# Optimization experiments

Measured on AMD Instinct MI355X. Metric: run time of the kernel, lower is better.

The kernel has to match this reference:

```python
import jax, jax.numpy as jnp
import numpy as np

DIM = 512
BLOCK = 64
SPARSITY = 0.9
B, L = 4, 2048
NEG_INF = jnp.float32(-jnp.inf)


def _block_sparse_mask(key, seq_len, block_size, sparsity):
    # mirrors BasicQuantumAttention._get_block_sparse_mask, with diagonal
    # blocks forced on so no softmax row is fully masked (avoids NaNs)
    nb = (seq_len + block_size - 1) // block_size
    blk = jax.random.uniform(key, (nb, nb)) > sparsity
    blk = jnp.tril(blk) | jnp.eye(nb, dtype=bool)
    m = jnp.repeat(jnp.repeat(blk, block_size, axis=0), block_size, axis=1)
    return m[:seq_len, :seq_len]


def setup_inputs() -> dict:
    key = jax.random.key(0)
    ks = jax.random.split(key, 12)
    d = DIM
    inp = {}
    names = ['q_real', 'q_imag', 'k_real', 'k_imag', 'v_real', 'v_imag']
    for i, n in enumerate(names):
        inp[n] = jax.random.normal(ks[i], (B, L, d), dtype=jnp.float32)
    # xavier-ish init for Linear weights (torch Linear: y = x @ W.T + b)
    s6 = (2.0 / (6 * d + 6 * d)) ** 0.5
    s2 = (2.0 / (2 * d + 2 * d)) ** 0.5
    inp['W_qkv'] = jax.random.normal(ks[6], (6 * d, 6 * d), dtype=jnp.float32) * s6
    inp['b_qkv'] = jnp.zeros((6 * d,), dtype=jnp.float32)
    inp['W_out'] = jax.random.normal(ks[7], (2 * d, 2 * d), dtype=jnp.float32) * s2
    inp['b_out'] = jnp.zeros((2 * d,), dtype=jnp.float32)
    # two independent random block-sparse masks (one per stream, as in the
    # original which regenerates the mask inside each _chunk_attention call)
    inp['mask_real'] = _block_sparse_mask(ks[8], L, BLOCK, SPARSITY)
    inp['mask_imag'] = _block_sparse_mask(ks[9], L, BLOCK, SPARSITY)
    return inp


def _masked_attention(q, k, v, mask, scale):
    # q,k,v: [B,L,d]; mask: [L,L] bool (True = keep)
    scores = jnp.einsum('bqd,bkd->bqk', q, k) * scale
    scores = jnp.where(mask[None, :, :], scores, NEG_INF)
    attn = jax.nn.softmax(scores, axis=-1)  # dropout is identity in eval
    return jnp.einsum('bqk,bkd->bqd', attn, v)


def reference(q_real, q_imag, k_real, k_imag, v_real, v_imag,
              W_qkv, b_qkv, W_out, b_out, mask_real, mask_imag):
    d = q_real.shape[-1]
    scale = jnp.asarray(d, q_real.dtype) ** -0.5
    x = jnp.concatenate([q_real, q_imag, k_real, k_imag, v_real, v_imag], axis=-1)
    qkv = x @ W_qkv.T + b_qkv                       # [B,L,6d]
    q_r, q_i, k_r, k_i, v_r, v_i = jnp.split(qkv, 6, axis=-1)
    out_real = _masked_attention(q_r, k_r, v_r, mask_real, scale)
    out_imag = _masked_attention(q_i, k_i, v_i, mask_imag, scale)
    out = jnp.concatenate([out_real, out_imag], axis=-1)  # [B,L,2d]
    out = out @ W_out.T + b_out
    return out[..., :d], out[..., d:]
```

## Files before the change

### kernel.cpp

```cpp
#include <hip/hip_runtime.h>
#include <stdint.h>

typedef __attribute__((ext_vector_type(8))) short short8;
typedef __attribute__((ext_vector_type(4))) float f32x4;

#define DEV __device__ __forceinline__

DEV unsigned short f2bf(float f) {
    unsigned int u = __float_as_uint(f);
    u += 0x7FFFu + ((u >> 16) & 1u);
    return (unsigned short)(u >> 16);
}

DEV void gload_lds16(const void* g, void* l) {
    __builtin_amdgcn_global_load_lds(
        (const __attribute__((address_space(1))) unsigned int*)g,
        (__attribute__((address_space(3))) unsigned int*)l,
        16, 0, 0);
}

__global__ __launch_bounds__(256) void f32_to_bf16_k(
    const float* __restrict__ in, unsigned short* __restrict__ out, int n8) {
    int i = blockIdx.x * 256 + threadIdx.x;
    if (i >= n8) return;
    const float4* src = (const float4*)in + (size_t)i * 2;
    float4 a = src[0], b = src[1];
    short8 o;
    o[0] = f2bf(a.x); o[1] = f2bf(a.y); o[2] = f2bf(a.z); o[3] = f2bf(a.w);
    o[4] = f2bf(b.x); o[5] = f2bf(b.y); o[6] = f2bf(b.z); o[7] = f2bf(b.w);
    *((short8*)out + i) = o;
}

__global__ __launch_bounds__(256) void pack_x_k(
    const float* __restrict__ p0, const float* __restrict__ p1,
    const float* __restrict__ p2, const float* __restrict__ p3,
    const float* __restrict__ p4, const float* __restrict__ p5,
    unsigned short* __restrict__ x) {
    int i = blockIdx.x * 256 + threadIdx.x;
    int e0 = i * 8;
    int m = e0 / 3072;
    int k = e0 - m * 3072;
    int sel = k >> 9;
    const float* src;
    switch (sel) {
        case 0: src = p0; break; case 1: src = p1; break;
        case 2: src = p2; break; case 3: src = p3; break;
        case 4: src = p4; break; default: src = p5; break;
    }
    src += (size_t)m * 512 + (k & 511);
    float4 a = *(const float4*)src;
    float4 b = *(const float4*)(src + 4);
    short8 o;
    o[0] = f2bf(a.x); o[1] = f2bf(a.y); o[2] = f2bf(a.z); o[3] = f2bf(a.w);
    o[4] = f2bf(b.x); o[5] = f2bf(b.y); o[6] = f2bf(b.z); o[7] = f2bf(b.w);
    *(short8*)(x + e0) = o;
}

__global__ void scan_masks_k(const void* mr, const void* mi,
                             int* __restrict__ nact, unsigned char* __restrict__ lists) {
    int t = threadIdx.x;
    if (t >= 64) return;
    int s = t >> 5, qb = t & 31;
    const unsigned char* det = (const unsigned char*)mr;
    bool is_byte = det[1] != 0;
    const void* m = s ? mi : mr;
    int cnt = 0;
    for (int kb = 0; kb < 32; ++kb) {
        size_t off = (size_t)(qb * 64) * 2048 + (size_t)kb * 64;
        bool on = is_byte ? (((const unsigned char*)m)[off] != 0)
                          : (((const int*)m)[off] != 0);
        if (on) lists[t * 32 + cnt++] = (unsigned char)kb;
    }
    nact[t] = cnt;
}

template <int MODE>
__global__ __launch_bounds__(256, 2) void gemm_bt(
    const unsigned short* __restrict__ A, const unsigned short* __restrict__ B,
    const float* __restrict__ bias, unsigned short* __restrict__ Cb,
    float* __restrict__ Cf, int M, int N, int K, int halfN, int half_elems) {
    __shared__ unsigned short As[128 * 32];
    __shared__ unsigned short Bs[128 * 32];
    const int tid = threadIdx.x;
    const int wave = tid >> 6, lane = tid & 63;
    const int bm = blockIdx.x, bn = blockIdx.y;
    const int wr = wave >> 1, wc = wave & 1;
    const int fr = lane & 15, fo = lane >> 4;
    const int srow = lane >> 2;
    const int scol = (lane & 3) * 8;
    f32x4 acc[4][4];
    #pragma unroll
    for (int mi = 0; mi < 4; ++mi)
        #pragma unroll
        for (int ni = 0; ni < 4; ++ni) acc[mi][ni] = f32x4{0.f, 0.f, 0.f, 0.f};

    for (int k0 = 0; k0 < K; k0 += 32) {
        #pragma unroll
        for (int r = 0; r < 2; ++r) {
            int arow = bm * 128 + r * 64 + wave * 16 + srow;
            gload_lds16(A + (size_t)arow * K + k0 + scol,
                        As + (r * 64 + wave * 16) * 32);
            int brow = bn * 128 + r * 64 + wave * 16 + srow;
            gload_lds16(B + (size_t)brow * K + k0 + scol,
                        Bs + (r * 64 + wave * 16) * 32);
        }
        __syncthreads();
        short8 af[4], bfr[4];
        #pragma unroll
        for (int mi = 0; mi < 4; ++mi)
            af[mi] = *(const short8*)(As + (wr * 64 + mi * 16 + fr) * 32 + fo * 8);
        #pragma unroll
        for (int ni = 0; ni < 4; ++ni)
            bfr[ni] = *(const short8*)(Bs + (wc * 64 + ni * 16 + fr) * 32 + fo * 8);
        #pragma unroll
        for (int mi = 0; mi < 4; ++mi)
            #pragma unroll
            for (int ni = 0; ni < 4; ++ni)
                acc[mi][ni] = __builtin_amdgcn_mfma_f32_16x16x32_bf16(
                    af[mi], bfr[ni], acc[mi][ni], 0, 0, 0);
        __syncthreads();
    }
    #pragma unroll
    for (int mi = 0; mi < 4; ++mi)
        #pragma unroll
        for (int ni = 0; ni < 4; ++ni)
            #pragma unroll
            for (int j = 0; j < 4; ++j) {
                int gr = bm * 128 + wr * 64 + mi * 16 + fo * 4 + j;
                int gc = bn * 128 + wc * 64 + ni * 16 + fr;
                float v = acc[mi][ni][j] + bias[gc];
                if (MODE == 0) {
                    Cb[(size_t)gr * N + gc] = f2bf(v);
                } else {
                    if (gc < halfN) Cf[(size_t)gr * halfN + gc] = v;
                    else Cf[half_elems + (size_t)gr * halfN + (gc - halfN)] = v;
                }
            }
}

__global__ __launch_bounds__(256) void transpose_v_k(
    const unsigned short* __restrict__ qkv, unsigned short* __restrict__ Vt) {
    int idx = blockIdx.x;
    int kt = idx & 31; idx >>= 5;
    int dt = idx & 7;  idx >>= 3;
    int b  = idx & 3;  idx >>= 2;
    int s  = idx;
    __shared__ unsigned short tile[64][65];
    int t = threadIdx.x;
    int r = t >> 2;
    int cs = (t & 3) * 16;
    const unsigned short* src =
        qkv + (size_t)(b * 2048 + kt * 64 + r) * 3072 + 2048 + s * 512 + dt * 64 + cs;
    short8 v0 = *(const short8*)src;
    short8 v1 = *(const short8*)(src + 8);
    #pragma unroll
    for (int i = 0; i < 8; ++i) { tile[r][cs + i] = v0[i]; tile[r][cs + 8 + i] = v1[i]; }
    __syncthreads();
    short8 o0, o1;
    #pragma unroll
    for (int i = 0; i < 8; ++i) { o0[i] = tile[cs + i][r]; o1[i] = tile[cs + 8 + i][r]; }
    unsigned short* dst =
        Vt + (size_t)((s * 4 + b) * 512 + dt * 64 + r) * 2048 + kt * 64 + cs;
    *(short8*)dst = o0;
    *(short8*)(dst + 8) = o1;
}

__global__ __launch_bounds__(256, 1) void attn_k(
    const unsigned short* __restrict__ qkv, const unsigned short* __restrict__ Vt,
    unsigned short* __restrict__ attn, const int* __restrict__ nact,
    const unsigned char* __restrict__ lists) {
    int wg = blockIdx.x;
    int swz = (wg & 7) * 32 + (wg >> 3);
    int b = swz >> 6, s = (swz >> 5) & 1, qb = swz & 31;
    int wave = threadIdx.x >> 6, lane = threadIdx.x & 63;
    int fr = lane & 15, fo = lane >> 4;
    const float scale = 0.04419417382415922f;
    __shared__ unsigned short Pl[4][1024];
    unsigned char* Plb = (unsigned char*)&Pl[wave][0];

    int qoff = s * 512, koff = 1024 + s * 512;
    size_t vtbase = (size_t)((s * 4 + b) * 512) * 2048;
    int mrow = b * 2048 + qb * 64 + wave * 16;

    short8 qf[16];
    const unsigned short* qrow_ptr = qkv + (size_t)(mrow + fr) * 3072 + qoff + fo * 8;
    #pragma unroll
    for (int kk = 0; kk < 16; ++kk) qf[kk] = *(const short8*)(qrow_ptr + kk * 32);

    f32x4 acc[32];
    #pragma unroll
    for (int di = 0; di < 32; ++di) acc[di] = f32x4{0.f, 0.f, 0.f, 0.f};
    float mr[4] = {-1e30f, -1e30f, -1e30f, -1e30f};
    float lr[4] = {0.f, 0.f, 0.f, 0.f};

    int na = nact[s * 32 + qb];
    const unsigned char* lst = lists + (s * 32 + qb) * 32;

    for (int t = 0; t < na; ++t) {
        int kb = lst[t];
        const unsigned short* kbase_ptr =
            qkv + (size_t)(b * 2048 + kb * 64 + fr) * 3072 + koff + fo * 8;
        f32x4 sf[4];
        #pragma unroll
        for (int nf = 0; nf < 4; ++nf) {
            sf[nf] = f32x4{0.f, 0.f, 0.f, 0.f};
            const unsigned short* kp = kbase_ptr + (size_t)nf * 16 * 3072;
            #pragma unroll
            for (int kk = 0; kk < 16; ++kk) {
                short8 kf = *(const short8*)(kp + kk * 32);
                sf[nf] = __builtin_amdgcn_mfma_f32_16x16x32_bf16(qf[kk], kf, sf[nf], 0, 0, 0);
            }
        }
        #pragma unroll
        for (int nf = 0; nf < 4; ++nf) sf[nf] *= scale;
        float bm[4], f_[4], rs[4];
        #pragma unroll
        for (int j = 0; j < 4; ++j) {
            float v = fmaxf(fmaxf(sf[0][j], sf[1][j]), fmaxf(sf[2][j], sf[3][j]));
            #pragma unroll
            for (int off = 1; off < 16; off <<= 1) v = fmaxf(v, __shfl_xor(v, off, 64));
            bm[j] = v;
        }
        #pragma unroll
        for (int j = 0; j < 4; ++j) {
            float mn = fmaxf(mr[j], bm[j]);
            f_[j] = __expf(mr[j] - mn);
            mr[j] = mn;
            rs[j] = 0.f;
        }
        #pragma unroll
        for (int nf = 0; nf < 4; ++nf)
            #pragma unroll
            for (int j = 0; j < 4; ++j) {
                float p = __expf(sf[nf][j] - mr[j]);
                sf[nf][j] = p;
                rs[j] += p;
            }
        #pragma unroll
        for (int j = 0; j < 4; ++j) {
            float v = rs[j];
            #pragma unroll
            for (int off = 1; off < 16; off <<= 1) v += __shfl_xor(v, off, 64);
            lr[j] = lr[j] * f_[j] + v;
        }
        #pragma unroll
        for (int di = 0; di < 32; ++di) {
            acc[di][0] *= f_[0]; acc[di][1] *= f_[1];
            acc[di][2] *= f_[2]; acc[di][3] *= f_[3];
        }
        #pragma unroll
        for (int nf = 0; nf < 4; ++nf)
            #pragma unroll
            for (int j = 0; j < 4; ++j) {
                int row = fo * 4 + j, col = nf * 16 + fr;
                int byte = row * 128 + ((col * 2) ^ ((row & 7) << 4));
                *(unsigned short*)(Plb + byte) = f2bf(sf[nf][j]);
            }
        asm volatile("s_waitcnt lgkmcnt(0)" ::: "memory");
        #pragma unroll
        for (int ks = 0; ks < 2; ++ks) {
            int rbyte = fr * 128 + (((ks * 32 + fo * 8) * 2) ^ ((fr & 7) << 4));
            short8 pf = *(const short8*)(Plb + rbyte);
            const unsigned short* vp =
                Vt + vtbase + (size_t)fr * 2048 + kb * 64 + ks * 32 + fo * 8;
            #pragma unroll
            for (int di = 0; di < 32; ++di) {
                short8 vf = *(const short8*)(vp + (size_t)di * 16 * 2048);
                acc[di] = __builtin_amdgcn_mfma_f32_16x16x32_bf16(pf, vf, acc[di], 0, 0, 0);
            }
        }
    }
    float inv[4];
    #pragma unroll
    for (int j = 0; j < 4; ++j) inv[j] = 1.0f / lr[j];
    unsigned short* orow = attn + (size_t)(mrow + fo * 4) * 1024 + s * 512 + fr;
    #pragma unroll
    for (int di = 0; di < 32; ++di)
        #pragma unroll
        for (int j = 0; j < 4; ++j)
            orow[(size_t)j * 1024 + di * 16] = f2bf(acc[di][j] * inv[j]);
}

extern "C" void kernel_launch(void* const* d_in, const int* in_sizes, int n_in,
                              void* d_out, int out_size, void* d_ws, size_t ws_size,
                              hipStream_t stream) {
    const float* q_r = (const float*)d_in[0];
    const float* q_i = (const float*)d_in[1];
    const float* k_r = (const float*)d_in[2];
    const float* k_i = (const float*)d_in[3];
    const float* v_r = (const float*)d_in[4];
    const float* v_i = (const float*)d_in[5];
    const float* W_qkv = (const float*)d_in[6];
    const float* b_qkv = (const float*)d_in[7];
    const float* W_out = (const float*)d_in[8];
    const float* b_out = (const float*)d_in[9];
    const void* mask_r = d_in[10];
    const void* mask_i = d_in[11];

    char* ws = (char*)d_ws;
    unsigned short* x    = (unsigned short*)(ws);
    unsigned short* Wq   = (unsigned short*)(ws + 50331648);
    unsigned short* qkv  = (unsigned short*)(ws + 69206016);
    unsigned short* Wo   = (unsigned short*)(ws + 119537664);
    int* nact            = (int*)(ws + 121634816);
    unsigned char* lists = (unsigned char*)(ws + 121634816 + 256);
    unsigned short* Vt   = x;
    unsigned short* attn = x + 8388608;

    f32_to_bf16_k<<<4608, 256, 0, stream>>>(W_qkv, Wq, 1179648);
    f32_to_bf16_k<<<512, 256, 0, stream>>>(W_out, Wo, 131072);
    pack_x_k<<<12288, 256, 0, stream>>>(q_r, q_i, k_r, k_i, v_r, v_i, x);
    scan_masks_k<<<1, 64, 0, stream>>>(mask_r, mask_i, nact, lists);
    gemm_bt<0><<<dim3(64, 24), 256, 0, stream>>>(x, Wq, b_qkv, qkv, nullptr,
                                                 8192, 3072, 3072, 0, 0);
    transpose_v_k<<<2048, 256, 0, stream>>>(qkv, Vt);
    attn_k<<<256, 256, 0, stream>>>(qkv, Vt, attn, nact, lists);
    gemm_bt<1><<<dim3(64, 8), 256, 0, stream>>>(attn, Wo, b_out, nullptr,
                                                (float*)d_out, 8192, 1024, 1024,
                                                512, 4194304);
}
```

Measured before the change: 561.9 us.

## Replace GEMM with 256x256 double-buffered swizzled kernel and split attention per wave

Replaces the 128x128 single-buffered GEMM with a 256x256-tile, 512-thread kernel. It double-buffers 64-wide K tiles in XOR-swizzled LDS, uses explicit barrier/setprio phases to overlap global loads with MFMA work, and maps workgroups to XCDs. The attention kernel is split into 1024 single-wave workgroups instead of 256 four-wave ones, to raise parallelism and spread work across CUs. The risks are fewer GEMM workgroups (128 for the output projection), which leaves CUs idle, and reuse of K/V across query quarters in LDS or L2.

```diff
diff --git a/kernel.cpp b/kernel.cpp
--- a/kernel.cpp
+++ b/kernel.cpp
@@ -74,60 +74,132 @@
     nact[t] = cnt;
 }
 
+
+#define MFMA16(mbase)                                                          \
+    do {                                                                       \
+        _Pragma("unroll")                                                      \
+        for (int m_ = 0; m_ < 4; ++m_) {                                       \
+            _Pragma("unroll")                                                  \
+            for (int n_ = 0; n_ < 4; ++n_)                                     \
+                acc[(mbase) + m_][n_] = __builtin_amdgcn_mfma_f32_16x16x32_bf16( \
+                    af[m_], bf[n_], acc[(mbase) + m_][n_], 0, 0, 0);           \
+        }                                                                      \
+    } while (0)
+
+#define PHASE_PRE()                                          \
+    __builtin_amdgcn_s_barrier();                            \
+    asm volatile("s_waitcnt lgkmcnt(0)" ::: "memory");       \
+    __builtin_amdgcn_sched_barrier(0);                       \
+    __builtin_amdgcn_s_setprio(1)
+
+#define PHASE_END()                                          \
+    __builtin_amdgcn_s_setprio(0);                           \
+    __builtin_amdgcn_s_barrier();                            \
+    asm volatile("" ::: "memory")
+
+#define PHASE_END_V4()                                       \
+    __builtin_amdgcn_s_setprio(0);                           \
+    asm volatile("s_waitcnt vmcnt(4)" ::: "memory");         \
+    __builtin_amdgcn_s_barrier();                            \
+    asm volatile("" ::: "memory")
+
 template <int MODE>
-__global__ __launch_bounds__(256, 2) void gemm_bt(
+__global__ __launch_bounds__(512, 2) void gemm256(
     const unsigned short* __restrict__ A, const unsigned short* __restrict__ B,
     const float* __restrict__ bias, unsigned short* __restrict__ Cb,
-    float* __restrict__ Cf, int M, int N, int K, int halfN, int half_elems) {
-    __shared__ unsigned short As[128 * 32];
-    __shared__ unsigned short Bs[128 * 32];
+    float* __restrict__ Cf, int M, int N, int K, int NBN, int halfN, int half_elems) {
+    __shared__ unsigned short lds[2][4][8192];
     const int tid = threadIdx.x;
-    const int wave = tid >> 6, lane = tid & 63;
-    const int bm = blockIdx.x, bn = blockIdx.y;
-    const int wr = wave >> 1, wc = wave & 1;
-    const int fr = lane & 15, fo = lane >> 4;
-    const int srow = lane >> 2;
-    const int scol = (lane & 3) * 8;
-    f32x4 acc[4][4];
-    #pragma unroll
-    for (int mi = 0; mi < 4; ++mi)
-        #pragma unroll
-        for (int ni = 0; ni < 4; ++ni) acc[mi][ni] = f32x4{0.f, 0.f, 0.f, 0.f};
-
-    for (int k0 = 0; k0 < K; k0 += 32) {
-        #pragma unroll
-        for (int r = 0; r < 2; ++r) {
-            int arow = bm * 128 + r * 64 + wave * 16 + srow;
-            gload_lds16(A + (size_t)arow * K + k0 + scol,
-                        As + (r * 64 + wave * 16) * 32);
-            int brow = bn * 128 + r * 64 + wave * 16 + srow;
-            gload_lds16(B + (size_t)brow * K + k0 + scol,
-                        Bs + (r * 64 + wave * 16) * 32);
-        }
-        __syncthreads();
-        short8 af[4], bfr[4];
-        #pragma unroll
-        for (int mi = 0; mi < 4; ++mi)
-            af[mi] = *(const short8*)(As + (wr * 64 + mi * 16 + fr) * 32 + fo * 8);
+    const int wv = tid >> 6, ln = tid & 63;
+    const int fr = ln & 15, fo = ln >> 4;
+    const int wr = wv >> 2, wc = wv & 3;
+    const int cpx = gridDim.x >> 3;
+    const int wgid = (blockIdx.x & 7) * cpx + (blockIdx.x >> 3);
+    const int bm = wgid / NBN, bn = wgid % NBN;
+    const unsigned short* Abase = A + (size_t)(bm * 256) * K;
+    const unsigned short* Bbase = B + (size_t)(bn * 256) * K;
+    const int NT = K >> 6;
+    const int NI = NT >> 1;
+
+    auto stagePair = [&](int buf, int isB, int t) {
+        const unsigned short* G = isB ? Bbase : Abase;
+        unsigned short* Ld = &lds[buf][isB ? 2 : 0][0];
+        const int kcol = t * 64;
+        #pragma unroll
+        for (int r2 = 0; r2 < 4; ++r2) {
+            int d = r2 * 8192 + wv * 1024 + ln * 16;
+            int s = d ^ (((d >> 7) & 7) << 4);
+            int grow = s >> 7;
+            int gcol = (s & 127) >> 1;
+            gload_lds16(G + (size_t)grow * K + kcol + gcol,
+                        (char*)Ld + r2 * 8192 + wv * 1024);
+        }
+    };
+    auto readA = [&](int buf, int mh, int ks, short8* dst) {
+        #pragma unroll
+        for (int m = 0; m < 4; ++m) {
+            int row = wr * 128 + mh * 64 + m * 16 + fr;
+            int byte = (row * 128 + ks * 64 + fo * 16) ^ ((row & 7) << 4);
+            dst[m] = *(const short8*)((const char*)&lds[buf][0][0] + byte);
+        }
+    };
+    auto readB = [&](int buf, int ks, short8* dst) {
+        #pragma unroll
+        for (int n = 0; n < 4; ++n) {
+            int row = wc * 64 + n * 16 + fr;
+            int byte = (row * 128 + ks * 64 + fo * 16) ^ ((row & 7) << 4);
+            dst[n] = *(const short8*)((const char*)&lds[buf][2][0] + byte);
+        }
+    };
+
+    f32x4 acc[8][4];
+    #pragma unroll
+    for (int m = 0; m < 8; ++m)
+        #pragma unroll
+        for (int n = 0; n < 4; ++n) acc[m][n] = f32x4{0.f, 0.f, 0.f, 0.f};
+
+    stagePair(0, 0, 0);
+    stagePair(0, 1, 0);
+    stagePair(1, 1, 1);
+    asm volatile("s_waitcnt vmcnt(4)" ::: "memory");
+    __builtin_amdgcn_s_barrier();
+    asm volatile("" ::: "memory");
+
+    for (int i = 0; i < NI; ++i) {
+        const int t1 = 2 * i + 1;
+        const int tn0 = (2 * i + 2) % NT;
+        const int tn1 = (2 * i + 3) % NT;
+        short8 af[4], bf[4];
+        readA(0, 0, 0, af); readB(0, 0, bf);
+        stagePair(1, 0, t1);
+        PHASE_PRE(); MFMA16(0); PHASE_END();
+        readA(0, 1, 0, af);
+        PHASE_PRE(); MFMA16(4); PHASE_END();
+        readA(0, 0, 1, af); readB(0, 1, bf);
+        PHASE_PRE(); MFMA16(0); PHASE_END();
+        readA(0, 1, 1, af);
+        stagePair(0, 1, tn0);
+        PHASE_PRE(); MFMA16(4); PHASE_END_V4();
+        readA(1, 0, 0, af); readB(1, 0, bf);
+        stagePair(0, 0, tn0);
+        PHASE_PRE(); MFMA16(0); PHASE_END();
+        readA(1, 1, 0, af);
+        PHASE_PRE(); MFMA16(4); PHASE_END();
+        readA(1, 0, 1, af); readB(1, 1, bf);
+        PHASE_PRE(); MFMA16(0); PHASE_END();
+        readA(1, 1, 1, af);
+        stagePair(1, 1, tn1);
+        PHASE_PRE(); MFMA16(4); PHASE_END_V4();
+    }
+
+    #pragma unroll
+    for (int mi = 0; mi < 8; ++mi)
         #pragma unroll
         for (int ni = 0; ni < 4; ++ni)
-            bfr[ni] = *(const short8*)(Bs + (wc * 64 + ni * 16 + fr) * 32 + fo * 8);
-        #pragma unroll
-        for (int mi = 0; mi < 4; ++mi)
-            #pragma unroll
-            for (int ni = 0; ni < 4; ++ni)
-                acc[mi][ni] = __builtin_amdgcn_mfma_f32_16x16x32_bf16(
-                    af[mi], bfr[ni], acc[mi][ni], 0, 0, 0);
-        __syncthreads();
-    }
-    #pragma unroll
-    for (int mi = 0; mi < 4; ++mi)
-        #pragma unroll
-        for (int ni = 0; ni < 4; ++ni)
             #pragma unroll
             for (int j = 0; j < 4; ++j) {
-                int gr = bm * 128 + wr * 64 + mi * 16 + fo * 4 + j;
-                int gc = bn * 128 + wc * 64 + ni * 16 + fr;
+                int gr = bm * 256 + wr * 128 + mi * 16 + fo * 4 + j;
+                int gc = bn * 256 + wc * 64 + ni * 16 + fr;
                 float v = acc[mi][ni][j] + bias[gc];
                 if (MODE == 0) {
                     Cb[(size_t)gr * N + gc] = f2bf(v);
@@ -165,22 +237,23 @@
     *(short8*)(dst + 8) = o1;
 }
 
-__global__ __launch_bounds__(256, 1) void attn_k(
+__global__ __launch_bounds__(64) void attn_k(
     const unsigned short* __restrict__ qkv, const unsigned short* __restrict__ Vt,
     unsigned short* __restrict__ attn, const int* __restrict__ nact,
     const unsigned char* __restrict__ lists) {
     int wg = blockIdx.x;
-    int swz = (wg & 7) * 32 + (wg >> 3);
-    int b = swz >> 6, s = (swz >> 5) & 1, qb = swz & 31;
-    int wave = threadIdx.x >> 6, lane = threadIdx.x & 63;
+    int xcd = wg & 7, idx = wg >> 3;
+    int b = xcd >> 1, s = xcd & 1;
+    int qb = idx >> 2, quarter = idx & 3;
+    int lane = threadIdx.x;
     int fr = lane & 15, fo = lane >> 4;
     const float scale = 0.04419417382415922f;
-    __shared__ unsigned short Pl[4][1024];
-    unsigned char* Plb = (unsigned char*)&Pl[wave][0];
+    __shared__ unsigned short Pl[1024];
+    unsigned char* Plb = (unsigned char*)&Pl[0];
 
     int qoff = s * 512, koff = 1024 + s * 512;
     size_t vtbase = (size_t)((s * 4 + b) * 512) * 2048;
-    int mrow = b * 2048 + qb * 64 + wave * 16;
+    int mrow = b * 2048 + qb * 64 + quarter * 16;
 
     short8 qf[16];
     const unsigned short* qrow_ptr = qkv + (size_t)(mrow + fr) * 3072 + qoff + fo * 8;
@@ -311,11 +384,10 @@
     f32_to_bf16_k<<<512, 256, 0, stream>>>(W_out, Wo, 131072);
     pack_x_k<<<12288, 256, 0, stream>>>(q_r, q_i, k_r, k_i, v_r, v_i, x);
     scan_masks_k<<<1, 64, 0, stream>>>(mask_r, mask_i, nact, lists);
-    gemm_bt<0><<<dim3(64, 24), 256, 0, stream>>>(x, Wq, b_qkv, qkv, nullptr,
-                                                 8192, 3072, 3072, 0, 0);
+    gemm256<0><<<384, 512, 0, stream>>>(x, Wq, b_qkv, qkv, nullptr,
+                                        8192, 3072, 3072, 12, 0, 0);
     transpose_v_k<<<2048, 256, 0, stream>>>(qkv, Vt);
-    attn_k<<<256, 256, 0, stream>>>(qkv, Vt, attn, nact, lists);
-    gemm_bt<1><<<dim3(64, 8), 256, 0, stream>>>(attn, Wo, b_out, nullptr,
-                                                (float*)d_out, 8192, 1024, 1024,
-                                                512, 4194304);
-}
+    attn_k<<<1024, 64, 0, stream>>>(qkv, Vt, attn, nact, lists);
+    gemm256<1><<<128, 512, 0, stream>>>(attn, Wo, b_out, nullptr, (float*)d_out,
+                                        8192, 1024, 1024, 4, 512, 4194304);
+}
```

Result: faster. 531.4 us (-5.4%).
